# Kernel optimization log

Hardware: AMD Instinct MI355X
Metric: run time of the kernel (lower is better)

## Reference

```python
import jax, jax.numpy as jnp
import numpy as np

NEIGHBOR_NUM = 4
POOLING_RATE = 4


def setup_inputs() -> dict:
    key = jax.random.key(0)
    k1, k2, k3 = jax.random.split(key, 3)
    B, N, C = 4, 8192, 256
    vertices = jax.random.normal(k1, (B, N, 3), dtype=jnp.float32)
    feature_map = jax.random.normal(k2, (B, N, C), dtype=jnp.float32)
    pool_num = N // POOLING_RATE
    sample_idx = jax.random.permutation(k3, N)[:pool_num].astype(jnp.int32)  # torch.randperm(N)[:pool_num]
    return {"vertices": vertices, "feature_map": feature_map, "radius": 1, "sample_idx": sample_idx}


def _query_ball_point(radius, nsample, xyz):
    # xyz: [B, N, 3]; self-query (new_xyz == xyz)
    B, N, _ = xyz.shape
    sq = jnp.sum(xyz * xyz, axis=-1)                       # [B, N]
    dist = -2.0 * jnp.einsum('bnc,bmc->bnm', xyz, xyz)     # [B, N, N]
    dist = dist + sq[:, :, None] + sq[:, None, :]
    # original code zeroes the diagonal (self-distance)
    diag = jnp.arange(N)
    dist = dist.at[:, diag, diag].set(0.0)
    # mark out-of-ball entries with sentinel N, sort indices, keep first nsample
    idx = jnp.arange(N, dtype=jnp.int32)
    group_idx = jnp.where(dist > radius ** 2, jnp.int32(N), idx[None, None, :])  # [B, N, N]
    group_idx = jnp.sort(group_idx, axis=-1)[:, :, :nsample]                     # [B, N, nsample]
    group_first = group_idx[:, :, :1]
    group_idx = jnp.where(group_idx == N, group_first, group_idx)
    return group_idx


def reference(vertices, feature_map, radius, sample_idx):
    B, N, _ = vertices.shape
    neighbor_index = _query_ball_point(radius, NEIGHBOR_NUM, vertices)          # [B, N, k]
    bidx = jnp.arange(B)[:, None, None]
    neighbor_feature = feature_map[bidx, neighbor_index]                        # [B, N, k, C]
    pooled_feature = jnp.max(neighbor_feature, axis=2)                          # [B, N, C]
    vertices_pool = vertices[:, sample_idx, :]                                  # [B, pool, 3]
    feature_map_pool = pooled_feature[:, sample_idx, :]                         # [B, pool, C]
    return (vertices_pool, feature_map_pool)
```

## Files before the change

kernel.cpp:

```cpp
#include <hip/hip_runtime.h>


#define BB 4
#define NN 8192
#define CC 256
#define PP 2048
#define KK 4
#define CH1 8
#define CH2 16
#define R2ROUNDS (NN / (64 * CH2))

__device__ __forceinline__ float dist_ref(float xn0, float xn1, float xn2, float sqn,
                                          float x0, float x1, float x2) {
    const float sqm = __fadd_rn(__fadd_rn(__fmul_rn(x0, x0), __fmul_rn(x1, x1)),
                                __fmul_rn(x2, x2));
    const float dot = __fadd_rn(__fadd_rn(__fmul_rn(xn0, x0), __fmul_rn(xn1, x1)),
                                __fmul_rn(xn2, x2));
    return __fadd_rn(__fadd_rn(__fmul_rn(-2.0f, dot), sqn), sqm);
}

__global__ __launch_bounds__(256) void pool_layer_kernel(
    const float* __restrict__ vertices,
    const float* __restrict__ feat,
    const int*   __restrict__ radius_p,
    const int*   __restrict__ sample_idx,
    float* __restrict__ out_v,
    float* __restrict__ out_f)
{
    const int wave = threadIdx.x >> 6;
    const int lane = threadIdx.x & 63;
    const int q    = blockIdx.x * 4 + wave;
    const int b    = q >> 11;
    const int i    = q & (PP - 1);
    const float* vb = vertices + (size_t)b * NN * 3;

    float px[CH1], py[CH1], pz[CH1];
    #pragma unroll
    for (int c = 0; c < CH1; ++c) {
        const int m = c * 64 + lane;
        px[c] = vb[m * 3 + 0];
        py[c] = vb[m * 3 + 1];
        pz[c] = vb[m * 3 + 2];
    }

    const int n = sample_idx[i];
    const float xn0 = vb[n * 3 + 0];
    const float xn1 = vb[n * 3 + 1];
    const float xn2 = vb[n * 3 + 2];
    const float sqn = __fadd_rn(__fadd_rn(__fmul_rn(xn0, xn0), __fmul_rn(xn1, xn1)),
                                __fmul_rn(xn2, xn2));
    const int   r  = radius_p[0];
    const float r2 = (float)(r * r);

    if (lane < 3) out_v[((size_t)b * PP + i) * 3 + lane] = vb[n * 3 + lane];

    int c0 = 0, c1 = 0, c2 = 0, c3 = 0, cnt = 0;
    #pragma unroll
    for (int c = 0; c < CH1; ++c) {
        const int m = c * 64 + lane;
        const float dist = dist_ref(xn0, xn1, xn2, sqn, px[c], py[c], pz[c]);
        unsigned long long mask = __ballot((m == n) || !(dist > r2));
        while (mask && cnt < KK) {
            const int v = c * 64 + (__ffsll(mask) - 1);
            c3 = (cnt == 3) ? v : c3;
            c2 = (cnt == 2) ? v : c2;
            c1 = (cnt == 1) ? v : c1;
            c0 = (cnt == 0) ? v : c0;
            ++cnt;
            mask &= (mask - 1);
        }
    }

    if (cnt < KK) {
        int l0 = NN, l1 = NN, l2 = NN, l3 = NN, lcnt = 0;
        for (int base = 0; base < NN; base += 64 * CH2) {
            float qx[CH2], qy[CH2], qz[CH2];
            #pragma unroll
            for (int c = 0; c < CH2; ++c) {
                const int m = base + c * 64 + lane;
                qx[c] = vb[m * 3 + 0];
                qy[c] = vb[m * 3 + 1];
                qz[c] = vb[m * 3 + 2];
            }
            #pragma unroll
            for (int c = 0; c < CH2; ++c) {
                const int m = base + c * 64 + lane;
                const float dist = dist_ref(xn0, xn1, xn2, sqn, qx[c], qy[c], qz[c]);
                const bool hit = (m == n) || !(dist > r2);
                if (hit && lcnt < KK) {
                    l3 = (lcnt == 3) ? m : l3;
                    l2 = (lcnt == 2) ? m : l2;
                    l1 = (lcnt == 1) ? m : l1;
                    l0 = (lcnt == 0) ? m : l0;
                    ++lcnt;
                }
            }
        }
        int g[KK];
        #pragma unroll
        for (int round = 0; round < KK; ++round) {
            int mmin = l0;
            #pragma unroll
            for (int off = 32; off > 0; off >>= 1)
                mmin = min(mmin, __shfl_xor(mmin, off));
            g[round] = mmin;
            if (l0 == mmin) { l0 = l1; l1 = l2; l2 = l3; l3 = NN; }
        }
        c0 = g[0];
        c1 = (g[1] == NN) ? g[0] : g[1];
        c2 = (g[2] == NN) ? g[0] : g[2];
        c3 = (g[3] == NN) ? g[0] : g[3];
    }

    const float4 a0 = ((const float4*)(feat + ((size_t)b * NN + c0) * CC))[lane];
    const float4 a1 = ((const float4*)(feat + ((size_t)b * NN + c1) * CC))[lane];
    const float4 a2 = ((const float4*)(feat + ((size_t)b * NN + c2) * CC))[lane];
    const float4 a3 = ((const float4*)(feat + ((size_t)b * NN + c3) * CC))[lane];
    float4 o;
    o.x = fmaxf(fmaxf(a0.x, a1.x), fmaxf(a2.x, a3.x));
    o.y = fmaxf(fmaxf(a0.y, a1.y), fmaxf(a2.y, a3.y));
    o.z = fmaxf(fmaxf(a0.z, a1.z), fmaxf(a2.z, a3.z));
    o.w = fmaxf(fmaxf(a0.w, a1.w), fmaxf(a2.w, a3.w));
    ((float4*)(out_f + ((size_t)b * PP + i) * CC))[lane] = o;
}

extern "C" void kernel_launch(void* const* d_in, const int* in_sizes, int n_in,
                              void* d_out, int out_size, void* d_ws, size_t ws_size,
                              hipStream_t stream) {
    const float* vertices   = (const float*)d_in[0];
    const float* feat       = (const float*)d_in[1];
    const int*   radius_p   = (const int*)d_in[2];
    const int*   sample_idx = (const int*)d_in[3];

    float* out_v = (float*)d_out;
    float* out_f = out_v + (size_t)BB * PP * 3;

    dim3 grid(BB * PP / 4), block(256);
    pool_layer_kernel<<<grid, block, 0, stream>>>(
        vertices, feat, radius_p, sample_idx, out_v, out_f);
}
```

Before: 96.93 us.

## Stage first 1024 vertices in LDS and early-exit the fallback scan

Each block now cooperatively loads the first 1024 vertices into shared memory with float4 loads and scans them in the first pass, instead of each wave loading 512 vertices into registers. This widens the fast path so fewer queries fall back to the full 8192-point scan. The fallback loop also counts hits with a ballot and popcount and stops once at least four neighbours are found. The change adds a block-wide barrier and 12 KB of LDS per block, which may reduce occupancy.

```diff
diff --git a/kernel.cpp b/kernel.cpp
--- a/kernel.cpp
+++ b/kernel.cpp
@@ -6,9 +6,8 @@
 #define CC 256
 #define PP 2048
 #define KK 4
-#define CH1 8
+#define SS 1024
 #define CH2 16
-#define R2ROUNDS (NN / (64 * CH2))
 
 __device__ __forceinline__ float dist_ref(float xn0, float xn1, float xn2, float sqn,
                                           float x0, float x1, float x2) {
@@ -27,21 +26,20 @@
     float* __restrict__ out_v,
     float* __restrict__ out_f)
 {
-    const int wave = threadIdx.x >> 6;
-    const int lane = threadIdx.x & 63;
+    __shared__ float s_v[SS * 3];
+
+    const int tid  = threadIdx.x;
+    const int wave = tid >> 6;
+    const int lane = tid & 63;
     const int q    = blockIdx.x * 4 + wave;
     const int b    = q >> 11;
     const int i    = q & (PP - 1);
     const float* vb = vertices + (size_t)b * NN * 3;
 
-    float px[CH1], py[CH1], pz[CH1];
-    #pragma unroll
-    for (int c = 0; c < CH1; ++c) {
-        const int m = c * 64 + lane;
-        px[c] = vb[m * 3 + 0];
-        py[c] = vb[m * 3 + 1];
-        pz[c] = vb[m * 3 + 2];
-    }
+    const float4* v4 = (const float4*)vb;
+    const float4 st0 = v4[tid];
+    const float4 st1 = v4[tid + 256];
+    const float4 st2 = v4[tid + 512];
 
     const int n = sample_idx[i];
     const float xn0 = vb[n * 3 + 0];
@@ -52,13 +50,22 @@
     const int   r  = radius_p[0];
     const float r2 = (float)(r * r);
 
+    ((float4*)s_v)[tid]       = st0;
+    ((float4*)s_v)[tid + 256] = st1;
+    ((float4*)s_v)[tid + 512] = st2;
+
     if (lane < 3) out_v[((size_t)b * PP + i) * 3 + lane] = vb[n * 3 + lane];
+
+    __syncthreads();
 
     int c0 = 0, c1 = 0, c2 = 0, c3 = 0, cnt = 0;
     #pragma unroll
-    for (int c = 0; c < CH1; ++c) {
+    for (int c = 0; c < SS / 64; ++c) {
         const int m = c * 64 + lane;
-        const float dist = dist_ref(xn0, xn1, xn2, sqn, px[c], py[c], pz[c]);
+        const float x0 = s_v[m * 3 + 0];
+        const float x1 = s_v[m * 3 + 1];
+        const float x2 = s_v[m * 3 + 2];
+        const float dist = dist_ref(xn0, xn1, xn2, sqn, x0, x1, x2);
         unsigned long long mask = __ballot((m == n) || !(dist > r2));
         while (mask && cnt < KK) {
             const int v = c * 64 + (__ffsll(mask) - 1);
@@ -73,7 +80,8 @@
 
     if (cnt < KK) {
         int l0 = NN, l1 = NN, l2 = NN, l3 = NN, lcnt = 0;
-        for (int base = 0; base < NN; base += 64 * CH2) {
+        int tot = 0;
+        for (int base = 0; base < NN && tot < KK; base += 64 * CH2) {
             float qx[CH2], qy[CH2], qz[CH2];
             #pragma unroll
             for (int c = 0; c < CH2; ++c) {
@@ -87,6 +95,7 @@
                 const int m = base + c * 64 + lane;
                 const float dist = dist_ref(xn0, xn1, xn2, sqn, qx[c], qy[c], qz[c]);
                 const bool hit = (m == n) || !(dist > r2);
+                tot += (int)__popcll(__ballot(hit));
                 if (hit && lcnt < KK) {
                     l3 = (lcnt == 3) ? m : l3;
                     l2 = (lcnt == 2) ? m : l2;
```

New measurement: 97.76 us. Within noise of the previous version (+0.9%).
